# Kernel tuning notes

Measured on AMD Instinct MI355X. Metric: run time of the kernel, lower is better.

The kernel has to match this reference:

```python
import jax, jax.numpy as jnp
import numpy as np

BN_EPS = 1e-5
LEAKY_SLOPE = 0.2


def setup_inputs() -> dict:
    key = jax.random.key(0)
    k1, k2 = jax.random.split(key, 2)
    B, C, N, O = 8, 64, 4096, 64
    data = jax.random.normal(k1, (B, C, N), dtype=jnp.float32)
    # 1x1 Conv2d(channels_in=2C, channels_out=O, bias=False) kernel -> [O, 2C]
    W = jax.random.normal(k2, (O, 2 * C), dtype=jnp.float32) * 0.05
    gamma = jnp.ones((O,), dtype=jnp.float32)
    beta = jnp.zeros((O,), dtype=jnp.float32)
    return {"data": data, "W": W, "gamma": gamma, "beta": beta, "k": 20}


def reference(data, W, gamma, beta, k):
    B, C, N = data.shape
    xt = jnp.transpose(data, (0, 2, 1))                 # [B, N, C]
    # knn via -||xi - xj||^2 = -xx - 2*(-x.x) - xx  (topk of negative sq dist)
    inner = -2.0 * jnp.matmul(xt, data)                 # [B, N, N]
    xx = jnp.sum(data * data, axis=1)                   # [B, N]
    pdist = -xx[:, :, None] - inner - xx[:, None, :]    # [B, N, N]
    idx = jax.lax.top_k(pdist, k)[1]                    # [B, N, k] int32
    # gather neighbor features: [B, N, k, C]
    feat = jax.vmap(lambda d, i: d[i])(xt, idx)
    center = xt[:, :, None, :]                          # [B, N, 1, C]
    edge = jnp.concatenate(
        [feat - center, jnp.broadcast_to(center, (B, N, k, C))], axis=-1
    )                                                   # [B, N, k, 2C]
    # 1x1 conv == channel matmul -> [B, O, N, k]
    y = jnp.einsum('bnkc,oc->bonk', edge, W)
    # BatchNorm2d, training-mode batch stats over (B, N, k) per channel
    mean = jnp.mean(y, axis=(0, 2, 3), keepdims=True)
    var = jnp.mean((y - mean) ** 2, axis=(0, 2, 3), keepdims=True)
    y = (y - mean) * jax.lax.rsqrt(var + BN_EPS)
    y = y * gamma[None, :, None, None] + beta[None, :, None, None]
    # LeakyReLU(0.2)
    y = jnp.where(y >= 0, y, LEAKY_SLOPE * y)
    # max over k neighbors -> [B, O, N]
    return jnp.max(y, axis=-1)
```

## Files before the change

kernel.cpp:

```cpp
#include <hip/hip_runtime.h>
#include <hip/hip_fp16.h>
#include <float.h>

#define B 8
#define C 64
#define N 4096
#define O 64
#define KMAX 32
#define NREP 64

typedef unsigned short u16;
typedef unsigned int u32;
typedef unsigned long long u64;
typedef __attribute__((ext_vector_type(8))) u16 u16x8;
typedef __attribute__((ext_vector_type(8))) short bf16x8;
typedef __attribute__((ext_vector_type(4))) float f32x4;

__device__ __forceinline__ u16 f2bf(float f) {
    unsigned u = __builtin_bit_cast(unsigned, f);
    unsigned r = (u + 0x7FFFu + ((u >> 16) & 1)) >> 16;
    return (u16)r;
}

__global__ __launch_bounds__(256) void ec_prep(const float* __restrict__ x,
                                               const float* __restrict__ W,
                                               float* __restrict__ xx,
                                               float* __restrict__ xt,
                                               u16* __restrict__ xtb,
                                               __half* __restrict__ u,
                                               __half* __restrict__ v) {
    __shared__ float xs[64][65];
    __shared__ float W1[C][64];
    __shared__ float Wd[C][64];
    __shared__ float rs[4][64];
    const int blk = blockIdx.x;
    const int b = blk >> 6;
    const int n0 = (blk & 63) << 6;
    const int t = threadIdx.x;
#pragma unroll
    for (int p = 0; p < 16; ++p) {
        int q = t + 256 * p; int c = q >> 6, j = q & 63;
        xs[c][j] = x[(size_t)b * C * N + (size_t)c * N + n0 + j];
    }
#pragma unroll
    for (int p = 0; p < 16; ++p) {
        int q = t + 256 * p; int c = q >> 6, o = q & 63;
        float w1 = W[o * 128 + c];
        float w2 = W[o * 128 + 64 + c];
        W1[c][o] = w1; Wd[c][o] = w2 - w1;
    }
    __syncthreads();
    {
        const int j = t >> 2, g = t & 3;
        float vals[16]; float ss = 0.f;
#pragma unroll
        for (int i = 0; i < 16; ++i) { float f = xs[g * 16 + i][j]; vals[i] = f; ss += f * f; }
        rs[g][j] = ss;
        size_t rowb = ((size_t)b * N + n0 + j) * 64 + g * 16;
#pragma unroll
        for (int i = 0; i < 4; ++i) {
            float4 v4 = { vals[4 * i], vals[4 * i + 1], vals[4 * i + 2], vals[4 * i + 3] };
            *(float4*)&xt[rowb + 4 * i] = v4;
        }
        u16x8 h0, h1;
#pragma unroll
        for (int i = 0; i < 8; ++i) { h0[i] = f2bf(vals[i]); h1[i] = f2bf(vals[8 + i]); }
        *(u16x8*)&xtb[rowb] = h0;
        *(u16x8*)&xtb[rowb + 8] = h1;
    }
    {
        const int o = t & 63, ji = t >> 6;
        float su[16] = {}, sv[16] = {};
#pragma unroll 1
        for (int c = 0; c < C; ++c) {
            float w1 = W1[c][o];
            float wd = Wd[c][o];
#pragma unroll
            for (int p = 0; p < 16; ++p) {
                float xv = xs[c][ji + 4 * p];
                su[p] = fmaf(xv, w1, su[p]);
                sv[p] = fmaf(xv, wd, sv[p]);
            }
        }
#pragma unroll
        for (int p = 0; p < 16; ++p) {
            size_t base = ((size_t)b * N + n0 + ji + 4 * p) * O + o;
            u[base] = __float2half(su[p]);
            v[base] = __float2half(sv[p]);
        }
    }
    __syncthreads();
    if (t < 64) xx[(size_t)b * N + t + n0] = rs[0][t] + rs[1][t] + rs[2][t] + rs[3][t];
}

#define CXD(a, b) { u32 mx_ = max(a, b); b = min(a, b); a = mx_; }
#define CXA(a, b) { u32 mn_ = min(a, b); b = max(a, b); a = mn_; }
#define BSORT8(e0,e1,e2,e3,e4,e5,e6,e7) { \
    CXD(e0,e1) CXA(e2,e3) CXD(e4,e5) CXA(e6,e7) \
    CXD(e0,e2) CXD(e1,e3) CXA(e4,e6) CXA(e5,e7) \
    CXD(e0,e1) CXD(e2,e3) CXA(e4,e5) CXA(e6,e7) \
    CXD(e0,e4) CXD(e1,e5) CXD(e2,e6) CXD(e3,e7) \
    CXD(e0,e2) CXD(e1,e3) CXD(e4,e6) CXD(e5,e7) \
    CXD(e0,e1) CXD(e2,e3) CXD(e4,e5) CXD(e6,e7) }
#define MERGETOP8(t0,t1,t2,t3,t4,t5,t6,t7, e0,e1,e2,e3,e4,e5,e6,e7) { \
    t0 = max(t0, e7); t1 = max(t1, e6); t2 = max(t2, e5); t3 = max(t3, e4); \
    t4 = max(t4, e3); t5 = max(t5, e2); t6 = max(t6, e1); t7 = max(t7, e0); \
    CXD(t0,t4) CXD(t1,t5) CXD(t2,t6) CXD(t3,t7) \
    CXD(t0,t2) CXD(t1,t3) CXD(t4,t6) CXD(t5,t7) \
    CXD(t0,t1) CXD(t2,t3) CXD(t4,t5) CXD(t6,t7) }

__global__ __launch_bounds__(256) void ec_gemm(const u16* __restrict__ xtb,
                                               const float* __restrict__ xx,
                                               u32* __restrict__ cand) {
    __shared__ u16 lds[18432 + 8];
    const int t = threadIdx.x;
    const int m0 = blockIdx.x * 128, n0 = blockIdx.y * 128;
    const int b = blockIdx.z;
    const u16* xa = xtb + (size_t)b * N * 64;
#pragma unroll
    for (int p = 0; p < 4; ++p) {
        int q = t + 256 * p;
        int row = q >> 3, ch = q & 7;
        int by = (row * 128 + ch * 16) ^ ((row & 7) << 4);
        *(u16x8*)((char*)lds + by) = *(const u16x8*)&xa[(size_t)(n0 + row) * 64 + ch * 8];
        *(u16x8*)((char*)lds + 16384 + by) = *(const u16x8*)&xa[(size_t)(m0 + row) * 64 + ch * 8];
    }
    __syncthreads();
    const int w = t >> 6, lane = t & 63;
    const int wr = w >> 1, wc = w & 1;
    const int fr = lane & 15, fg = lane >> 4;
    f32x4 acc[4][4] = {};
#pragma unroll
    for (int ks = 0; ks < 2; ++ks) {
        bf16x8 af[4], bg[4];
#pragma unroll
        for (int fi = 0; fi < 4; ++fi) {
            int rowA = 64 * wr + 16 * fi + fr;
            int byA = (rowA * 128 + ks * 64 + fg * 16) ^ ((rowA & 7) << 4);
            af[fi] = *(const bf16x8*)((const char*)lds + byA);
            int rowB = 64 * wc + 16 * fi + fr;
            int byB = (rowB * 128 + ks * 64 + fg * 16) ^ ((rowB & 7) << 4);
            bg[fi] = *(const bf16x8*)((const char*)lds + 16384 + byB);
        }
#pragma unroll
        for (int fi = 0; fi < 4; ++fi)
#pragma unroll
            for (int fj = 0; fj < 4; ++fj)
                acc[fi][fj] = __builtin_amdgcn_mfma_f32_16x16x32_bf16(af[fi], bg[fj], acc[fi][fj], 0, 0, 0);
    }
    float xmK[4];
#pragma unroll
    for (int fj = 0; fj < 4; ++fj)
        xmK[fj] = 2560.f - xx[(size_t)b * N + m0 + 64 * wc + 16 * fj + fr];
    __syncthreads();
    u16* ep = lds + w * 4608;
#pragma unroll
    for (int fi = 0; fi < 4; ++fi)
#pragma unroll
        for (int fj = 0; fj < 4; ++fj)
#pragma unroll
            for (int r = 0; r < 4; ++r) {
                float dvp = fmaf(2.f, acc[fi][fj][r], xmK[fj]);
                u32 bits = __builtin_bit_cast(u32, dvp);
                int row = 16 * fi + fg * 4 + r, col = 16 * fj + fr;
                ep[row * 72 + col] = (u16)(bits >> 7);
            }
    __syncthreads();
    const u16* myrow = lds + w * 4608 + lane * 72;
    const int mbase = m0 + (wc << 6);
    const u32 invb = (u32)(4095 - mbase);
    u32 t0, t1, t2, t3, t4, t5, t6, t7;
    {
        u16x8 q = *(const u16x8*)&myrow[0];
        t0 = ((u32)q[0] << 12) | (invb - 0); t1 = ((u32)q[1] << 12) | (invb - 1);
        t2 = ((u32)q[2] << 12) | (invb - 2); t3 = ((u32)q[3] << 12) | (invb - 3);
        t4 = ((u32)q[4] << 12) | (invb - 4); t5 = ((u32)q[5] << 12) | (invb - 5);
        t6 = ((u32)q[6] << 12) | (invb - 6); t7 = ((u32)q[7] << 12) | (invb - 7);
        BSORT8(t0, t1, t2, t3, t4, t5, t6, t7)
    }
#pragma unroll
    for (int g = 1; g < 8; ++g) {
        u16x8 q = *(const u16x8*)&myrow[g * 8];
        const u32 inv0 = invb - (u32)(g * 8);
        u32 e0 = ((u32)q[0] << 12) | (inv0 - 0), e1 = ((u32)q[1] << 12) | (inv0 - 1);
        u32 e2 = ((u32)q[2] << 12) | (inv0 - 2), e3 = ((u32)q[3] << 12) | (inv0 - 3);
        u32 e4 = ((u32)q[4] << 12) | (inv0 - 4), e5 = ((u32)q[5] << 12) | (inv0 - 5);
        u32 e6 = ((u32)q[6] << 12) | (inv0 - 6), e7 = ((u32)q[7] << 12) | (inv0 - 7);
        BSORT8(e0, e1, e2, e3, e4, e5, e6, e7)
        MERGETOP8(t0, t1, t2, t3, t4, t5, t6, t7, e0, e1, e2, e3, e4, e5, e6, e7)
    }
    __syncthreads();
    u32* mbuf = (u32*)lds;
    if (wc) {
        u32* mp = mbuf + (size_t)((wr << 6) | lane) * 8;
        uint4 w0 = { t0, t1, t2, t3 }, w1 = { t4, t5, t6, t7 };
        *(uint4*)mp = w0;
        *(uint4*)(mp + 4) = w1;
    }
    __syncthreads();
    if (!wc) {
        const u32* mp = mbuf + (size_t)((wr << 6) | lane) * 8;
        uint4 b0 = *(const uint4*)mp, b1 = *(const uint4*)(mp + 4);
        u32 e0 = b0.x, e1 = b0.y, e2 = b0.z, e3 = b0.w;
        u32 e4 = b1.x, e5 = b1.y, e6 = b1.z, e7 = b1.w;
        MERGETOP8(t0, t1, t2, t3, t4, t5, t6, t7, e0, e1, e2, e3, e4, e5, e6, e7)
        const int row_g = n0 + 64 * wr + lane;
        u32* cp = cand + (((size_t)b * N + row_g) * 32 + blockIdx.x) * 8;
        uint4 w0 = { t0, t1, t2, t3 }, w1 = { t4, t5, t6, t7 };
        *(uint4*)cp = w0;
        *(uint4*)(cp + 4) = w1;
    }
}

#define CX4(i, j) { u32 mn_ = min(c[i], c[j]); c[i] = max(c[i], c[j]); c[j] = mn_; }
#define CLEAN4IN() { CX4(0,2) CX4(1,3) CX4(0,1) CX4(2,3) }
#define DSTEP(xorm, bit) { \
    u32 pr_[4]; \
    _Pragma("unroll") for (int i_ = 0; i_ < 4; ++i_) pr_[i_] = __shfl_xor(c[i_], xorm); \
    bool km_ = (lane & (bit)) == 0; \
    _Pragma("unroll") for (int i_ = 0; i_ < 4; ++i_) \
        c[i_] = km_ ? max(c[i_], pr_[i_]) : min(c[i_], pr_[i_]); }

__global__ __launch_bounds__(256) void ec_sel(const u32* __restrict__ cand,
                                              const float* __restrict__ xt,
                                              const float* __restrict__ xx,
                                              const __half* __restrict__ u,
                                              const __half* __restrict__ v,
                                              const int* __restrict__ kptr,
                                              __half2* __restrict__ ext,
                                              float* __restrict__ statsR) {
    __shared__ float sxn[4][64];
    __shared__ int scand[4][32];
    __shared__ float rsum[256], rsum2[256];
    const int t = threadIdx.x, w = t >> 6, lane = t & 63;
    const int b = blockIdx.y;
    const int n = blockIdx.x * 4 + w;
    const int k = *kptr;

    const u32* cp = cand + (((size_t)b * N + n) * 32 + (lane >> 1)) * 8 + (lane & 1) * 4;
    uint4 a0 = *(const uint4*)cp;
    u32 c[4] = { a0.x, a0.y, a0.z, a0.w };

    {
        u32 pr[4];
#pragma unroll
        for (int i = 0; i < 4; ++i) pr[i] = __shfl_xor(c[3 - i], 3);
        bool lo = (lane & 2) == 0;
#pragma unroll
        for (int i = 0; i < 4; ++i) {
            u32 mx = max(c[i], pr[i]), mn = min(c[i], pr[i]);
            c[i] = lo ? mx : mn;
        }
        DSTEP(1, 1)
        CLEAN4IN()
    }
    {
        u32 pr[4];
#pragma unroll
        for (int i = 0; i < 4; ++i) pr[i] = __shfl_xor(c[3 - i], 7);
        bool lo = (lane & 4) == 0;
#pragma unroll
        for (int i = 0; i < 4; ++i) {
            u32 mx = max(c[i], pr[i]), mn = min(c[i], pr[i]);
            c[i] = lo ? mx : mn;
        }
        DSTEP(2, 2) DSTEP(1, 1)
        CLEAN4IN()
    }
#define MT32(mask) { \
        u32 pr_[4]; \
        _Pragma("unroll") for (int i_ = 0; i_ < 4; ++i_) pr_[i_] = __shfl_xor(c[3 - i_], mask); \
        _Pragma("unroll") for (int i_ = 0; i_ < 4; ++i_) c[i_] = max(c[i_], pr_[i_]); \
        DSTEP(4, 4) DSTEP(2, 2) DSTEP(1, 1) CLEAN4IN() }
    MT32(15)
    MT32(23)
    MT32(39)
#undef MT32

    if (lane < 8) {
#pragma unroll
        for (int i = 0; i < 4; ++i) scand[w][lane * 4 + i] = 4095 - (int)(c[i] & 0xFFFu);
    }
    sxn[w][lane] = xt[((size_t)b * N + n) * 64 + lane];
    __syncthreads();

    const float* xt_ = xt + (size_t)b * N * 64;
    const int jc = lane & 31, h = lane >> 5;
    const int mj = scand[w][jc];
    const float* xr = xt_ + (size_t)mj * 64 + h * 32;
    float acc = 0.f;
#pragma unroll
    for (int q8 = 0; q8 < 8; ++q8) {
        float4 g4 = *(const float4*)&xr[q8 * 4];
        float4 xn4 = *(const float4*)&sxn[w][h * 32 + q8 * 4];
        acc += g4.x * xn4.x + g4.y * xn4.y + g4.z * xn4.z + g4.w * xn4.w;
    }
    acc += __shfl_xor(acc, 32);
    float ex = 2.f * acc - xx[(size_t)b * N + mj];
    unsigned fu = __builtin_bit_cast(unsigned, ex);
    unsigned sf = fu ^ (unsigned)(((int)fu >> 31) | 0x80000000);
    u64 key = ((u64)sf << 12) | (u64)(4095 - mj);
    if (h) key = 0;

#pragma unroll
    for (int ls = 1; ls <= 5; ++ls) {
        const int s = 1 << ls;
        const bool lb = (lane & s) == 0;
#pragma unroll
        for (int dd = s >> 1; dd >= 1; dd >>= 1) {
            const bool km = ((lane & dd) == 0) == lb;
            u64 pv = __shfl_xor(key, dd);
            u64 mn = key < pv ? key : pv;
            u64 mx = key < pv ? pv : key;
            key = km ? mx : mn;
        }
    }
    int m_final = 4095 - (int)(key & 0xFFFu);

    const __half* ub = u + (size_t)b * N * O;
    size_t rowb = (size_t)b * N + n;
    float vv = __half2float(v[rowb * O + lane]);
    float gmax = -FLT_MAX, gmin = FLT_MAX, gs = 0.f, gs2 = 0.f;
    if (k == 20) {
        int mks[20];
#pragma unroll
        for (int kk = 0; kk < 20; ++kk) mks[kk] = __shfl(m_final, kk);
        float g[20];
#pragma unroll
        for (int kk = 0; kk < 20; ++kk)
            g[kk] = __half2float(ub[(size_t)mks[kk] * O + lane]);
#pragma unroll
        for (int kk = 0; kk < 20; ++kk) {
            gs += g[kk]; gs2 += g[kk] * g[kk];
            gmax = fmaxf(gmax, g[kk]); gmin = fminf(gmin, g[kk]);
        }
    } else {
        int mks[KMAX];
#pragma unroll
        for (int kk = 0; kk < KMAX; ++kk) mks[kk] = __shfl(m_final, kk);
        float g[KMAX];
#pragma unroll
        for (int kk = 0; kk < KMAX; ++kk)
            g[kk] = __half2float(ub[(size_t)mks[kk] * O + lane]);
#pragma unroll
        for (int kk = 0; kk < KMAX; ++kk) {
            if (kk < k) {
                gs += g[kk]; gs2 += g[kk] * g[kk];
                gmax = fmaxf(gmax, g[kk]); gmin = fminf(gmin, g[kk]);
            }
        }
    }
    float fk = (float)k;
    float s  = gs + fk * vv;
    float s2 = gs2 + 2.f * vv * gs + fk * vv * vv;
    ext[rowb * O + lane] = __halves2half2(__float2half(gmax + vv), __float2half(gmin + vv));
    rsum[t] = s; rsum2[t] = s2;
    __syncthreads();
    if (t < 64) {
        float a  = rsum[t] + rsum[t + 64] + rsum[t + 128] + rsum[t + 192];
        float a2 = rsum2[t] + rsum2[t + 64] + rsum2[t + 128] + rsum2[t + 192];
        float* sr = statsR + (size_t)(blockIdx.x & (NREP - 1)) * 128;
        atomicAdd(&sr[t], a);
        atomicAdd(&sr[64 + t], a2);
    }
}

__global__ void ec_final(const float* __restrict__ statsR,
                         const float* __restrict__ gamma,
                         const float* __restrict__ beta,
                         const int* __restrict__ kptr,
                         float* __restrict__ scsh) {
    int o = threadIdx.x;
    int k = *kptr;
    float s = 0.f, s2 = 0.f;
    for (int r = 0; r < NREP; ++r) {
        s  += statsR[r * 128 + o];
        s2 += statsR[r * 128 + 64 + o];
    }
    float M = (float)B * (float)N * (float)k;
    float mean = s / M;
    float var = s2 / M - mean * mean;
    var = fmaxf(var, 0.f);
    float sc = gamma[o] * rsqrtf(var + 1e-5f);
    float sh = beta[o] - mean * sc;
    scsh[o] = sc;
    scsh[64 + o] = sh;
}

__global__ __launch_bounds__(256) void ec_out(const __half2* __restrict__ ext,
                                              const float* __restrict__ scsh,
                                              float* __restrict__ out) {
    __shared__ float res[64][65];
    const int blk = blockIdx.x;
    const int b = blk >> 6;
    const int n0 = (blk & 63) << 6;
    const int t = threadIdx.x;
    {
        const int o = t & 63, ni = t >> 6;
        float sc = scsh[o], sh = scsh[64 + o];
#pragma unroll 1
        for (int p = 0; p < 16; ++p) {
            int nl = ni * 16 + p;
            size_t a = ((size_t)b * N + n0 + nl) * O + o;
            __half2 e = ext[a];
            float y = (sc >= 0.f) ? __low2float(e) : __high2float(e);
            float z = sc * y + sh;
            res[nl][o] = (z >= 0.f) ? z : 0.2f * z;
        }
    }
    __syncthreads();
    {
        const int j = t & 63, oi = t >> 6;
#pragma unroll 1
        for (int p = 0; p < 16; ++p) {
            int o2 = oi * 16 + p;
            out[(size_t)b * O * N + (size_t)o2 * N + n0 + j] = res[j][o2];
        }
    }
}

extern "C" void kernel_launch(void* const* d_in, const int* in_sizes, int n_in,
                              void* d_out, int out_size, void* d_ws, size_t ws_size,
                              hipStream_t stream) {
    const float* x     = (const float*)d_in[0];
    const float* W     = (const float*)d_in[1];
    const float* gamma = (const float*)d_in[2];
    const float* beta  = (const float*)d_in[3];
    const int*   kptr  = (const int*)d_in[4];
    float* out = (float*)d_out;

    char* ws = (char*)d_ws;
    u32*    cand = (u32*)ws;    ws += (size_t)B * N * 32 * 8 * 4;
    float*  xx   = (float*)ws;  ws += (size_t)B * N * 4;
    float*  xt   = (float*)ws;  ws += (size_t)B * N * C * 4;
    u16*    xtb  = (u16*)ws;    ws += (size_t)B * N * C * 2;
    __half* u_t  = (__half*)ws; ws += (size_t)B * N * O * 2;
    __half* v_t  = (__half*)ws; ws += (size_t)B * N * O * 2;
    __half2* ext = (__half2*)ws; ws += (size_t)B * N * O * 4;
    float* statsR = (float*)ws; ws += (size_t)NREP * 128 * 4;
    float* scsh  = (float*)ws;

    hipMemsetAsync(statsR, 0, NREP * 128 * 4, stream);
    ec_prep<<<B * N / 64, 256, 0, stream>>>(x, W, xx, xt, xtb, u_t, v_t);
    ec_gemm<<<dim3(N / 128, N / 128, B), 256, 0, stream>>>(xtb, xx, cand);
    ec_sel<<<dim3(N / 4, B), 256, 0, stream>>>(cand, xt, xx, u_t, v_t, kptr, ext, statsR);
    ec_final<<<1, 64, 0, stream>>>(statsR, gamma, beta, kptr, scsh);
    ec_out<<<B * N / 64, 256, 0, stream>>>(ext, scsh, out);
}
```

Measured before the change: 157.3 us.

## Halve prep tile to 32 points, pack weights as half2, use optimal 8-sort network

The prep kernel now processes 32 points per block instead of 64, doubling the grid to 1024 blocks and halving per-thread register accumulators. Weights are packed as half2 pairs in shared memory, which cuts LDS use but rounds the weights to fp16 before the u/v projection. The bitonic 8-element sort used in the gemm top-k is replaced with a 19-comparator optimal sorting network. These aim to improve occupancy in prep and trim compare-exchange work in the candidate selection, at the cost of some precision in the weights.

```diff
diff --git a/kernel.cpp b/kernel.cpp
--- a/kernel.cpp
+++ b/kernel.cpp
@@ -29,79 +29,81 @@
                                                u16* __restrict__ xtb,
                                                __half* __restrict__ u,
                                                __half* __restrict__ v) {
-    __shared__ float xs[64][65];
-    __shared__ float W1[C][64];
-    __shared__ float Wd[C][64];
-    __shared__ float rs[4][64];
+    __shared__ float xs[64][33];
+    __shared__ __half2 Wp[C][65];
+    __shared__ float rs[8][32];
     const int blk = blockIdx.x;
-    const int b = blk >> 6;
-    const int n0 = (blk & 63) << 6;
+    const int b = blk >> 7;
+    const int n0 = (blk & 127) << 5;
     const int t = threadIdx.x;
 #pragma unroll
+    for (int p = 0; p < 8; ++p) {
+        int q = t + 256 * p; int c = q >> 5, j = q & 31;
+        xs[c][j] = x[(size_t)b * C * N + (size_t)c * N + n0 + j];
+    }
+#pragma unroll
     for (int p = 0; p < 16; ++p) {
-        int q = t + 256 * p; int c = q >> 6, j = q & 63;
-        xs[c][j] = x[(size_t)b * C * N + (size_t)c * N + n0 + j];
-    }
-#pragma unroll
-    for (int p = 0; p < 16; ++p) {
-        int q = t + 256 * p; int c = q >> 6, o = q & 63;
+        int q = t + 256 * p; int o = q >> 6, c = q & 63;
         float w1 = W[o * 128 + c];
         float w2 = W[o * 128 + 64 + c];
-        W1[c][o] = w1; Wd[c][o] = w2 - w1;
-    }
-    __syncthreads();
-    {
-        const int j = t >> 2, g = t & 3;
-        float vals[16]; float ss = 0.f;
-#pragma unroll
-        for (int i = 0; i < 16; ++i) { float f = xs[g * 16 + i][j]; vals[i] = f; ss += f * f; }
+        Wp[c][o] = __floats2half2_rn(w1, w2 - w1);
+    }
+    __syncthreads();
+    {
+        const int j = t >> 3, g = t & 7;
+        float vals[8]; float ss = 0.f;
+#pragma unroll
+        for (int i = 0; i < 8; ++i) { float f = xs[g * 8 + i][j]; vals[i] = f; ss += f * f; }
         rs[g][j] = ss;
-        size_t rowb = ((size_t)b * N + n0 + j) * 64 + g * 16;
-#pragma unroll
-        for (int i = 0; i < 4; ++i) {
-            float4 v4 = { vals[4 * i], vals[4 * i + 1], vals[4 * i + 2], vals[4 * i + 3] };
-            *(float4*)&xt[rowb + 4 * i] = v4;
-        }
-        u16x8 h0, h1;
-#pragma unroll
-        for (int i = 0; i < 8; ++i) { h0[i] = f2bf(vals[i]); h1[i] = f2bf(vals[8 + i]); }
+        size_t rowb = ((size_t)b * N + n0 + j) * 64 + g * 8;
+        float4 v0 = { vals[0], vals[1], vals[2], vals[3] };
+        float4 v1 = { vals[4], vals[5], vals[6], vals[7] };
+        *(float4*)&xt[rowb] = v0;
+        *(float4*)&xt[rowb + 4] = v1;
+        u16x8 h0;
+#pragma unroll
+        for (int i = 0; i < 8; ++i) h0[i] = f2bf(vals[i]);
         *(u16x8*)&xtb[rowb] = h0;
-        *(u16x8*)&xtb[rowb + 8] = h1;
     }
     {
         const int o = t & 63, ji = t >> 6;
-        float su[16] = {}, sv[16] = {};
+        float su[8] = {}, sv[8] = {};
 #pragma unroll 1
         for (int c = 0; c < C; ++c) {
-            float w1 = W1[c][o];
-            float wd = Wd[c][o];
-#pragma unroll
-            for (int p = 0; p < 16; ++p) {
+            __half2 wp = Wp[c][o];
+            float w1 = __low2float(wp), wd = __high2float(wp);
+#pragma unroll
+            for (int p = 0; p < 8; ++p) {
                 float xv = xs[c][ji + 4 * p];
                 su[p] = fmaf(xv, w1, su[p]);
                 sv[p] = fmaf(xv, wd, sv[p]);
             }
         }
 #pragma unroll
-        for (int p = 0; p < 16; ++p) {
+        for (int p = 0; p < 8; ++p) {
             size_t base = ((size_t)b * N + n0 + ji + 4 * p) * O + o;
             u[base] = __float2half(su[p]);
             v[base] = __float2half(sv[p]);
         }
     }
     __syncthreads();
-    if (t < 64) xx[(size_t)b * N + t + n0] = rs[0][t] + rs[1][t] + rs[2][t] + rs[3][t];
+    if (t < 32) {
+        float a = 0.f;
+#pragma unroll
+        for (int g = 0; g < 8; ++g) a += rs[g][t];
+        xx[(size_t)b * N + n0 + t] = a;
+    }
 }
 
 #define CXD(a, b) { u32 mx_ = max(a, b); b = min(a, b); a = mx_; }
-#define CXA(a, b) { u32 mn_ = min(a, b); b = max(a, b); a = mn_; }
 #define BSORT8(e0,e1,e2,e3,e4,e5,e6,e7) { \
-    CXD(e0,e1) CXA(e2,e3) CXD(e4,e5) CXA(e6,e7) \
-    CXD(e0,e2) CXD(e1,e3) CXA(e4,e6) CXA(e5,e7) \
-    CXD(e0,e1) CXD(e2,e3) CXA(e4,e5) CXA(e6,e7) \
-    CXD(e0,e4) CXD(e1,e5) CXD(e2,e6) CXD(e3,e7) \
+    CXD(e0,e1) CXD(e2,e3) CXD(e4,e5) CXD(e6,e7) \
     CXD(e0,e2) CXD(e1,e3) CXD(e4,e6) CXD(e5,e7) \
-    CXD(e0,e1) CXD(e2,e3) CXD(e4,e5) CXD(e6,e7) }
+    CXD(e1,e2) CXD(e5,e6) CXD(e0,e4) CXD(e3,e7) \
+    CXD(e1,e5) CXD(e2,e6) \
+    CXD(e1,e4) CXD(e3,e6) \
+    CXD(e2,e4) CXD(e3,e5) \
+    CXD(e3,e4) }
 #define MERGETOP8(t0,t1,t2,t3,t4,t5,t6,t7, e0,e1,e2,e3,e4,e5,e6,e7) { \
     t0 = max(t0, e7); t1 = max(t1, e6); t2 = max(t2, e5); t3 = max(t3, e4); \
     t4 = max(t4, e3); t5 = max(t5, e2); t6 = max(t6, e1); t7 = max(t7, e0); \
@@ -441,7 +443,7 @@
     float* scsh  = (float*)ws;
 
     hipMemsetAsync(statsR, 0, NREP * 128 * 4, stream);
-    ec_prep<<<B * N / 64, 256, 0, stream>>>(x, W, xx, xt, xtb, u_t, v_t);
+    ec_prep<<<B * N / 32, 256, 0, stream>>>(x, W, xx, xt, xtb, u_t, v_t);
     ec_gemm<<<dim3(N / 128, N / 128, B), 256, 0, stream>>>(xtb, xx, cand);
     ec_sel<<<dim3(N / 4, B), 256, 0, stream>>>(cand, xt, xx, u_t, v_t, kptr, ext, statsR);
     ec_final<<<1, 64, 0, stream>>>(statsR, gamma, beta, kptr, scsh);
```

New measurement: 147.0 us. -6.5%, faster.
